# Optimization experiments

Measured on AMD Instinct MI355X. Metric: run time of the kernel, lower is better.

The kernel has to match this reference:

```python
import jax, jax.numpy as jnp
import numpy as np

B, T, K, NI, UNITS = 16, 512, 8, 256, 256


def hard_sigmoid(x):
    # Keras hard_sigmoid: clip(0.2*x + 0.5, 0, 1)
    return jnp.clip(0.2 * x + 0.5, 0.0, 1.0)


def setup_inputs() -> dict:
    key = jax.random.key(0)
    k1, k2, k3 = jax.random.split(key, 3)
    x = jax.random.normal(k1, (B, T, K, NI), dtype=jnp.float32)
    # glorot-ish scale for W, orthogonal-ish scale for U
    W = jax.random.normal(k2, (K, NI, 4 * UNITS), dtype=jnp.float32) * (1.0 / np.sqrt(NI))
    U = jax.random.normal(k3, (K, UNITS, 4 * UNITS), dtype=jnp.float32) * (1.0 / np.sqrt(UNITS))
    b = jnp.zeros((K, 4 * UNITS), dtype=jnp.float32)
    return {"x": x, "W": W, "U": U, "b": b}


def reference(x, W, U, b):
    units = W.shape[-1] // 4
    nb, nt, nk = x.shape[0], x.shape[1], x.shape[2]

    def step(carry, xt):
        h, c = carry  # [B, K, units]
        # grouped gate projections: per-kernel matmuls
        z = (jnp.einsum('bki,kij->bkj', xt, W)
             + jnp.einsum('bki,kij->bkj', h, U)
             + b)  # [B, K, 4*units]
        a = jnp.tanh(z[..., :units])
        i = hard_sigmoid(z[..., units:2 * units])
        f = hard_sigmoid(z[..., 2 * units:3 * units])
        o = hard_sigmoid(z[..., 3 * units:])
        c_new = a * i + f * c
        h_new = o * jnp.tanh(c_new)
        return (h_new, c_new), h_new

    h0 = jnp.zeros((nb, nk, units), x.dtype)
    c0 = jnp.zeros((nb, nk, units), x.dtype)
    (_, _), ys = jax.lax.scan(step, (h0, c0), jnp.swapaxes(x, 0, 1))  # ys: [T, B, K, units]
    return jnp.swapaxes(ys, 0, 1)  # [B, T, K, units]
```

## Files before the change

### kernel.cpp

```cpp
#include <hip/hip_runtime.h>
#include <cstdint>
#include <cstddef>

#define Tt  512
#define Kk  8
#define NI  256
#define UN  256
#define G4  1024

typedef unsigned short ushort_t;
typedef __attribute__((ext_vector_type(8))) short short8;
typedef __attribute__((ext_vector_type(4))) float f32x4;

__global__ void zero_ws(unsigned int* p, int n) {
    int stride = gridDim.x * blockDim.x;
    for (int i = blockIdx.x * blockDim.x + threadIdx.x; i < n; i += stride)
        p[i] = 0u;
}

__device__ __forceinline__ ushort_t f2bf(float x) {
    union { float f; unsigned int u; } v; v.f = x;
    unsigned int r = v.u + 0x7FFFu + ((v.u >> 16) & 1u);
    return (ushort_t)(r >> 16);
}

__device__ __forceinline__ float hsig(float z) {
    return fminf(1.0f, fmaxf(0.0f, fmaf(z, 0.2f, 0.5f)));
}

__device__ __forceinline__ float fast_tanh(float x) {
    float e = __expf(2.0f * x);
    return 1.0f - 2.0f * __builtin_amdgcn_rcpf(e + 1.0f);
}

__global__ __launch_bounds__(256) void xw_gemm(const float* __restrict__ x,
                                               const float* __restrict__ W,
                                               const float* __restrict__ bias,
                                               float* __restrict__ xw, int t0) {
    __shared__ __align__(16) float At[16][132];
    __shared__ __align__(16) float Bt[16][132];

    const int k  = blockIdx.z;
    const int C0 = blockIdx.x * 128;
    const int R0 = blockIdx.y * 128;
    const int tid = threadIdx.x;
    const int tx = tid & 15, ty = tid >> 4;

    float acc[8][8];
#pragma unroll
    for (int i = 0; i < 8; i++)
#pragma unroll
        for (int j = 0; j < 8; j++) acc[i][j] = 0.0f;

    const int lakk = tid & 15, larl = tid >> 4;
    const int lbc  = tid & 127, lbk = tid >> 7;

    for (int kt = 0; kt < NI; kt += 16) {
#pragma unroll
        for (int ps = 0; ps < 8; ps++) {
            int rloc = larl + ps * 16;
            int r = R0 + rloc;
            int b = r & 15, tp = r >> 4;
            At[lakk][rloc] = x[(((size_t)b * Tt + (t0 + tp)) * Kk + k) * NI + kt + lakk];
        }
#pragma unroll
        for (int ps = 0; ps < 8; ps++) {
            int kkr = lbk + ps * 2;
            Bt[kkr][lbc] = W[((size_t)k * NI + kt + kkr) * G4 + C0 + lbc];
        }
        __syncthreads();
#pragma unroll
        for (int kk = 0; kk < 16; kk++) {
            const float4* Ar = (const float4*)&At[kk][ty * 8];
            const float4* Br = (const float4*)&Bt[kk][tx * 8];
            float4 a0 = Ar[0], a1 = Ar[1];
            float4 b0 = Br[0], b1 = Br[1];
            float a[8] = {a0.x, a0.y, a0.z, a0.w, a1.x, a1.y, a1.z, a1.w};
            float bb[8] = {b0.x, b0.y, b0.z, b0.w, b1.x, b1.y, b1.z, b1.w};
#pragma unroll
            for (int i = 0; i < 8; i++)
#pragma unroll
                for (int j = 0; j < 8; j++)
                    acc[i][j] = fmaf(a[i], bb[j], acc[i][j]);
        }
        __syncthreads();
    }
    float bv[8];
#pragma unroll
    for (int j = 0; j < 8; j++) bv[j] = bias[(size_t)k * G4 + C0 + tx * 8 + j];
#pragma unroll
    for (int i = 0; i < 8; i++) {
        int r = R0 + ty * 8 + i;
        int b = r & 15, tp = r >> 4;
        float* op = xw + ((size_t)tp * 128 + b * 8 + k) * G4 + C0 + tx * 8;
#pragma unroll
        for (int j = 0; j < 8; j++) op[j] = acc[i][j] + bv[j];
    }
}

__global__ __launch_bounds__(256, 1) void lstm_mfma(
    const float* __restrict__ xw,
    const float* __restrict__ U,
    float* __restrict__ out,
    ushort_t* __restrict__ hstate,
    float* __restrict__ cstate,
    unsigned int* __restrict__ hbuf,
    int t0, int TC) {
    const int tid  = threadIdx.x;
    const int lane = tid & 63;
    const int w    = tid >> 6;
    const int k    = blockIdx.x & 7;
    const int uq   = blockIdx.x >> 3;
    const int l15  = lane & 15, quad = lane >> 4;

    __shared__ __align__(16) ushort_t hfr[2][4096];

    short8 bfr[4][8];
    const size_t Ubase = (size_t)k * (256 * 1024);
#pragma unroll
    for (int c = 0; c < 4; c++) {
        const int col = c * 256 + uq * 64 + w * 16 + l15;
#pragma unroll
        for (int q = 0; q < 8; q++) {
            short8 v;
#pragma unroll
            for (int j = 0; j < 8; j++) {
                int kk = q * 32 + quad * 8 + j;
                v[j] = (short)f2bf(U[Ubase + (size_t)kk * 1024 + col]);
            }
            bfr[c][q] = v;
        }
    }

    float cc[4];
    const size_t cbase = ((size_t)(k * 4 + uq)) * 1024 + (size_t)tid * 4;
#pragma unroll
    for (int r = 0; r < 4; r++) cc[r] = cstate[cbase + r];

    {
        const ushort_t* hs = hstate + (size_t)k * 4096;
#pragma unroll
        for (int i = 0; i < 16; i++) {
            int e = tid + 256 * i;
            int b = (e >> 6) & 15;
            int u = e & 63;
            int kkg = (e >> 10) * 64 + u;
            int q = kkg >> 5, j = kkg & 7;
            int c = q * 64 + (b + 16 * ((u & 31) >> 3));
            c ^= ((c >> 4) & 3) << 1;
            hfr[0][c * 8 + j] = hs[e];
        }
    }
    __syncthreads();

    const int colb = uq * 64 + w * 16 + l15;
    float xwv[4][4];
#pragma unroll
    for (int c = 0; c < 4; c++) {
#pragma unroll
        for (int r = 0; r < 4; r++) {
            int b = quad * 4 + r;
            xwv[c][r] = xw[((size_t)0 * 128 + b * 8 + k) * 1024 + c * 256 + colb];
        }
    }

    int p = 0;
#pragma unroll 1
    for (int t = 0; t < TC; t++) {
        const int g = t0 + t;

        short8 af[8];
#pragma unroll
        for (int q = 0; q < 8; q++) {
            int c = q * 64 + (lane ^ (quad << 1));
            af[q] = *(const short8*)&hfr[p][c * 8];
        }

        f32x4 acc[4];
        const f32x4 zv = {0.f, 0.f, 0.f, 0.f};
#pragma unroll
        for (int c = 0; c < 4; c++) acc[c] = zv;
#pragma unroll
        for (int q = 0; q < 8; q++) {
#pragma unroll
            for (int c = 0; c < 4; c++)
                acc[c] = __builtin_amdgcn_mfma_f32_16x16x32_bf16(af[q], bfr[c][q], acc[c], 0, 0, 0);
        }

        float hn[4];
#pragma unroll
        for (int r = 0; r < 4; r++) {
            float z0 = acc[0][r] + xwv[0][r];
            float z1 = acc[1][r] + xwv[1][r];
            float z2 = acc[2][r] + xwv[2][r];
            float z3 = acc[3][r] + xwv[3][r];
            float av = fast_tanh(z0);
            float iv = hsig(z1), fv = hsig(z2), ov = hsig(z3);
            float cn = av * iv + fv * cc[r];
            cc[r] = cn;
            hn[r] = ov * fast_tanh(cn);
        }

        if (t + 1 < TC) {
            const unsigned int tg = (unsigned int)(g + 1);
            unsigned int* dst = hbuf + ((size_t)((g + 1) & 1) * 8 + k) * 4096
                              + (size_t)uq * 1024 + w * 16 + l15;
#pragma unroll
            for (int r = 0; r < 4; r++) {
                unsigned int pv = ((unsigned int)f2bf(hn[r]) << 16) | tg;
                __hip_atomic_store(&dst[(quad * 4 + r) * 64], pv,
                                   __ATOMIC_RELAXED, __HIP_MEMORY_SCOPE_AGENT);
            }
            asm volatile("" ::: "memory");

#pragma unroll
            for (int r = 0; r < 4; r++) {
                int b = quad * 4 + r;
                out[(((size_t)b * Tt + g) * Kk + k) * UN + uq * 64 + w * 16 + l15] = hn[r];
            }

            float xwn[4][4];
#pragma unroll
            for (int c = 0; c < 4; c++)
#pragma unroll
                for (int r = 0; r < 4; r++) {
                    int b = quad * 4 + r;
                    xwn[c][r] = xw[((size_t)(t + 1) * 128 + b * 8 + k) * 1024 + c * 256 + colb];
                }

            const unsigned int* src = hbuf + ((size_t)((g + 1) & 1) * 8 + k) * 4096;
            unsigned int vals[16];
#pragma unroll
            for (int i = 0; i < 16; i++)
                vals[i] = __hip_atomic_load(&src[tid + 256 * i],
                                            __ATOMIC_RELAXED, __HIP_MEMORY_SCOPE_AGENT);
            for (;;) {
                bool ok = true;
#pragma unroll
                for (int i = 0; i < 16; i++) ok &= ((vals[i] & 0xFFFFu) == tg);
                if (ok) break;
#pragma unroll
                for (int i = 0; i < 16; i++)
                    vals[i] = __hip_atomic_load(&src[tid + 256 * i],
                                                __ATOMIC_RELAXED, __HIP_MEMORY_SCOPE_AGENT);
            }

            const int pn = p ^ 1;
#pragma unroll
            for (int i = 0; i < 16; i++) {
                int e = tid + 256 * i;
                int b = (e >> 6) & 15;
                int u = e & 63;
                int kkg = (e >> 10) * 64 + u;
                int q = kkg >> 5, j = kkg & 7;
                int c = q * 64 + (b + 16 * ((u & 31) >> 3));
                c ^= ((c >> 4) & 3) << 1;
                hfr[pn][c * 8 + j] = (ushort_t)(vals[i] >> 16);
            }
            __syncthreads();
            p = pn;
#pragma unroll
            for (int c = 0; c < 4; c++)
#pragma unroll
                for (int r = 0; r < 4; r++) xwv[c][r] = xwn[c][r];
        } else {
#pragma unroll
            for (int r = 0; r < 4; r++) {
                int b = quad * 4 + r;
                out[(((size_t)b * Tt + g) * Kk + k) * UN + uq * 64 + w * 16 + l15] = hn[r];
                hstate[(size_t)k * 4096 + (size_t)uq * 1024 + b * 64 + w * 16 + l15] = f2bf(hn[r]);
                cstate[cbase + r] = cc[r];
            }
        }
    }
}

extern "C" void kernel_launch(void* const* d_in, const int* in_sizes, int n_in,
                              void* d_out, int out_size, void* d_ws, size_t ws_size,
                              hipStream_t stream) {
    const float* x    = (const float*)d_in[0];
    const float* W    = (const float*)d_in[1];
    const float* U    = (const float*)d_in[2];
    const float* bias = (const float*)d_in[3];
    float* out = (float*)d_out;

    const size_t TAIL = 131072 + 65536 + 262144;
    int TC = 16;
    const int cands[6] = {512, 256, 128, 64, 32, 16};
    for (int ci = 0; ci < 6; ci++) {
        size_t need = (size_t)cands[ci] * 128 * 1024 * 4 + TAIL;
        if (need <= ws_size) { TC = cands[ci]; break; }
    }

    float* xw = (float*)d_ws;
    char* p = (char*)d_ws + (size_t)TC * 128 * 1024 * 4;
    float*        cstate = (float*)p;         p += 131072;
    ushort_t*     hstate = (ushort_t*)p;      p += 65536;
    unsigned int* hbuf   = (unsigned int*)p;

    zero_ws<<<dim3(128), dim3(256), 0, stream>>>((unsigned int*)cstate,
                                                 (int)(TAIL / 4));

    for (int t0 = 0; t0 < Tt; t0 += TC) {
        xw_gemm<<<dim3(G4 / 128, TC * 16 / 128, Kk), dim3(256), 0, stream>>>(
            x, W, bias, xw, t0);
        lstm_mfma<<<dim3(32), dim3(256), 0, stream>>>(
            xw, U, out, hstate, cstate, hbuf, t0, TC);
    }
}
```

Measured before the change: 1.379 ms.

## Split recurrent LSTM across two 512-thread blocks per kernel and overlap exchange with MFMA

```diff
diff --git a/kernel.cpp b/kernel.cpp
--- a/kernel.cpp
+++ b/kernel.cpp
@@ -31,6 +31,14 @@
 __device__ __forceinline__ float fast_tanh(float x) {
     float e = __expf(2.0f * x);
     return 1.0f - 2.0f * __builtin_amdgcn_rcpf(e + 1.0f);
+}
+
+__device__ __forceinline__ void lds_barrier() {
+    asm volatile("s_waitcnt lgkmcnt(0)" ::: "memory");
+    __builtin_amdgcn_sched_barrier(0);
+    __builtin_amdgcn_s_barrier();
+    __builtin_amdgcn_sched_barrier(0);
+    asm volatile("" ::: "memory");
 }
 
 __global__ __launch_bounds__(256) void xw_gemm(const float* __restrict__ x,
@@ -98,7 +106,7 @@
     }
 }
 
-__global__ __launch_bounds__(256, 1) void lstm_mfma(
+__global__ __launch_bounds__(512, 2) void lstm_mfma(
     const float* __restrict__ xw,
     const float* __restrict__ U,
     float* __restrict__ out,
@@ -110,7 +118,8 @@
     const int lane = tid & 63;
     const int w    = tid >> 6;
     const int k    = blockIdx.x & 7;
-    const int uq   = blockIdx.x >> 3;
+    const int uh   = blockIdx.x >> 3;
+    const int ph   = uh ^ 1;
     const int l15  = lane & 15, quad = lane >> 4;
 
     __shared__ __align__(16) ushort_t hfr[2][4096];
@@ -119,7 +128,7 @@
     const size_t Ubase = (size_t)k * (256 * 1024);
 #pragma unroll
     for (int c = 0; c < 4; c++) {
-        const int col = c * 256 + uq * 64 + w * 16 + l15;
+        const int col = c * 256 + uh * 128 + w * 16 + l15;
 #pragma unroll
         for (int q = 0; q < 8; q++) {
             short8 v;
@@ -133,27 +142,26 @@
     }
 
     float cc[4];
-    const size_t cbase = ((size_t)(k * 4 + uq)) * 1024 + (size_t)tid * 4;
+    const size_t cbase = ((size_t)(k * 2 + uh)) * 2048 + (size_t)tid * 4;
 #pragma unroll
     for (int r = 0; r < 4; r++) cc[r] = cstate[cbase + r];
 
     {
         const ushort_t* hs = hstate + (size_t)k * 4096;
 #pragma unroll
-        for (int i = 0; i < 16; i++) {
-            int e = tid + 256 * i;
-            int b = (e >> 6) & 15;
-            int u = e & 63;
-            int kkg = (e >> 10) * 64 + u;
-            int q = kkg >> 5, j = kkg & 7;
-            int c = q * 64 + (b + 16 * ((u & 31) >> 3));
-            c ^= ((c >> 4) & 3) << 1;
-            hfr[0][c * 8 + j] = hs[e];
+        for (int i = 0; i < 8; i++) {
+            int e = tid + 512 * i;
+            int b = (e >> 7) & 15;
+            int u = (e >> 11) * 128 + (e & 127);
+            int q = u >> 5, j = u & 7;
+            int ch = q * 64 + (b + 16 * ((u & 31) >> 3));
+            ch ^= ((ch >> 4) & 3) << 1;
+            hfr[0][ch * 8 + j] = hs[e];
         }
     }
     __syncthreads();
 
-    const int colb = uq * 64 + w * 16 + l15;
+    const int colb = uh * 128 + w * 16 + l15;
     float xwv[4][4];
 #pragma unroll
     for (int c = 0; c < 4; c++) {
@@ -169,11 +177,13 @@
     for (int t = 0; t < TC; t++) {
         const int g = t0 + t;
 
-        short8 af[8];
-#pragma unroll
-        for (int q = 0; q < 8; q++) {
-            int c = q * 64 + (lane ^ (quad << 1));
-            af[q] = *(const short8*)&hfr[p][c * 8];
+        const unsigned int* psrc = hbuf + ((size_t)(g & 1) * 8 + k) * 4096 + (size_t)ph * 2048;
+        unsigned int vals[4];
+        if (t > 0) {
+#pragma unroll
+            for (int i = 0; i < 4; i++)
+                vals[i] = __hip_atomic_load(&psrc[tid + 512 * i],
+                                            __ATOMIC_RELAXED, __HIP_MEMORY_SCOPE_AGENT);
         }
 
         f32x4 acc[4];
@@ -181,10 +191,48 @@
 #pragma unroll
         for (int c = 0; c < 4; c++) acc[c] = zv;
 #pragma unroll
-        for (int q = 0; q < 8; q++) {
+        for (int qq = 0; qq < 4; qq++) {
+            int q = uh * 4 + qq;
+            int ch = q * 64 + (lane ^ (quad << 1));
+            short8 af = *(const short8*)&hfr[p][ch * 8];
 #pragma unroll
             for (int c = 0; c < 4; c++)
-                acc[c] = __builtin_amdgcn_mfma_f32_16x16x32_bf16(af[q], bfr[c][q], acc[c], 0, 0, 0);
+                acc[c] = __builtin_amdgcn_mfma_f32_16x16x32_bf16(af, bfr[c][q], acc[c], 0, 0, 0);
+        }
+
+        if (t > 0) {
+            const unsigned int tg = (unsigned int)g;
+            for (;;) {
+                bool ok = true;
+#pragma unroll
+                for (int i = 0; i < 4; i++) ok &= ((vals[i] & 0xFFFFu) == tg);
+                if (ok) break;
+#pragma unroll
+                for (int i = 0; i < 4; i++)
+                    vals[i] = __hip_atomic_load(&psrc[tid + 512 * i],
+                                                __ATOMIC_RELAXED, __HIP_MEMORY_SCOPE_AGENT);
+            }
+#pragma unroll
+            for (int i = 0; i < 4; i++) {
+                int m = tid + 512 * i;
+                int b = m >> 7;
+                int u = ph * 128 + (m & 127);
+                int q = u >> 5, j = u & 7;
+                int ch = q * 64 + (b + 16 * ((u & 31) >> 3));
+                ch ^= ((ch >> 4) & 3) << 1;
+                hfr[p][ch * 8 + j] = (ushort_t)(vals[i] >> 16);
+            }
+            lds_barrier();
+        }
+
+#pragma unroll
+        for (int qq = 0; qq < 4; qq++) {
+            int q = ph * 4 + qq;
+            int ch = q * 64 + (lane ^ (quad << 1));
+            short8 af = *(const short8*)&hfr[p][ch * 8];
+#pragma unroll
+            for (int c = 0; c < 4; c++)
+                acc[c] = __builtin_amdgcn_mfma_f32_16x16x32_bf16(af, bfr[c][q], acc[c], 0, 0, 0);
         }
 
         float hn[4];
@@ -204,21 +252,34 @@
         if (t + 1 < TC) {
             const unsigned int tg = (unsigned int)(g + 1);
             unsigned int* dst = hbuf + ((size_t)((g + 1) & 1) * 8 + k) * 4096
-                              + (size_t)uq * 1024 + w * 16 + l15;
+                              + (size_t)uh * 2048 + w * 16 + l15;
 #pragma unroll
             for (int r = 0; r < 4; r++) {
                 unsigned int pv = ((unsigned int)f2bf(hn[r]) << 16) | tg;
-                __hip_atomic_store(&dst[(quad * 4 + r) * 64], pv,
+                __hip_atomic_store(&dst[(quad * 4 + r) * 128], pv,
                                    __ATOMIC_RELAXED, __HIP_MEMORY_SCOPE_AGENT);
             }
             asm volatile("" ::: "memory");
+
+            const int pn = p ^ 1;
+            {
+                const int u = uh * 128 + w * 16 + l15;
+                const int q = u >> 5, j = u & 7;
+                const int cpart = 16 * ((u & 31) >> 3);
+#pragma unroll
+                for (int r = 0; r < 4; r++) {
+                    int b = quad * 4 + r;
+                    int ch = q * 64 + b + cpart;
+                    ch ^= ((ch >> 4) & 3) << 1;
+                    hfr[pn][ch * 8 + j] = f2bf(hn[r]);
+                }
+            }
 
 #pragma unroll
             for (int r = 0; r < 4; r++) {
                 int b = quad * 4 + r;
-                out[(((size_t)b * Tt + g) * Kk + k) * UN + uq * 64 + w * 16 + l15] = hn[r];
-            }
-
+                out[(((size_t)b * Tt + g) * Kk + k) * UN + colb] = hn[r];
+            }
             float xwn[4][4];
 #pragma unroll
             for (int c = 0; c < 4; c++)
@@ -228,36 +289,7 @@
                     xwn[c][r] = xw[((size_t)(t + 1) * 128 + b * 8 + k) * 1024 + c * 256 + colb];
                 }
 
-            const unsigned int* src = hbuf + ((size_t)((g + 1) & 1) * 8 + k) * 4096;
-            unsigned int vals[16];
-#pragma unroll
-            for (int i = 0; i < 16; i++)
-                vals[i] = __hip_atomic_load(&src[tid + 256 * i],
-                                            __ATOMIC_RELAXED, __HIP_MEMORY_SCOPE_AGENT);
-            for (;;) {
-                bool ok = true;
-#pragma unroll
-                for (int i = 0; i < 16; i++) ok &= ((vals[i] & 0xFFFFu) == tg);
-                if (ok) break;
-#pragma unroll
-                for (int i = 0; i < 16; i++)
-                    vals[i] = __hip_atomic_load(&src[tid + 256 * i],
-                                                __ATOMIC_RELAXED, __HIP_MEMORY_SCOPE_AGENT);
-            }
-
-            const int pn = p ^ 1;
-#pragma unroll
-            for (int i = 0; i < 16; i++) {
-                int e = tid + 256 * i;
-                int b = (e >> 6) & 15;
-                int u = e & 63;
-                int kkg = (e >> 10) * 64 + u;
-                int q = kkg >> 5, j = kkg & 7;
-                int c = q * 64 + (b + 16 * ((u & 31) >> 3));
-                c ^= ((c >> 4) & 3) << 1;
-                hfr[pn][c * 8 + j] = (ushort_t)(vals[i] >> 16);
-            }
-            __syncthreads();
+            lds_barrier();
             p = pn;
 #pragma unroll
             for (int c = 0; c < 4; c++)
@@ -267,8 +299,8 @@
 #pragma unroll
             for (int r = 0; r < 4; r++) {
                 int b = quad * 4 + r;
-                out[(((size_t)b * Tt + g) * Kk + k) * UN + uq * 64 + w * 16 + l15] = hn[r];
-                hstate[(size_t)k * 4096 + (size_t)uq * 1024 + b * 64 + w * 16 + l15] = f2bf(hn[r]);
+                out[(((size_t)b * Tt + g) * Kk + k) * UN + colb] = hn[r];
+                hstate[(size_t)k * 4096 + (size_t)uh * 2048 + b * 128 + w * 16 + l15] = f2bf(hn[r]);
                 cstate[cbase + r] = cc[r];
             }
         }
@@ -304,7 +336,7 @@
     for (int t0 = 0; t0 < Tt; t0 += TC) {
         xw_gemm<<<dim3(G4 / 128, TC * 16 / 128, Kk), dim3(256), 0, stream>>>(
             x, W, bias, xw, t0);
-        lstm_mfma<<<dim3(32), dim3(256), 0, stream>>>(
+        lstm_mfma<<<dim3(16), dim3(512), 0, stream>>>(
             xw, U, out, hstate, cstate, hbuf, t0, TC);
     }
 }
```

After: 4.885 ms. 254% more time.
